# Kernel optimization log

Measured on AMD Instinct MI355X. Metric: run time of the kernel, lower is better.

The kernel has to match this reference:

```python
import jax, jax.numpy as jnp
import numpy as np

EPS = 1e-8
LAMBDA_LSE = 6.0
LAMBDA_SOFTMAX = 9.0
LEAKY_SLOPE = 0.1


def setup_inputs() -> dict:
    key = jax.random.key(0)
    k1, k2, k3 = jax.random.split(key, 3)
    images = jax.random.normal(k1, (128, 36, 512), dtype=jnp.float32)
    captions = jax.random.normal(k2, (64, 32, 512), dtype=jnp.float32)
    # caption lengths in [4, 32] so no caption is empty
    cap_lens = jax.random.randint(k3, (64,), 4, 33, dtype=jnp.int64)
    return {"images": images, "captions": captions, "cap_lens": cap_lens}


def reference(images, captions, cap_lens):
    """Vectorized xattn_score_t2i with raw_feature_norm='clipped_l2norm',
    agg_func='LogSumExp'. images: (I,R,D); captions: (C,L,D); cap_lens: (C,).
    Returns similarities (I, C), matching the torch per-caption loop.
    """
    C, L, D = captions.shape
    mask = jnp.arange(L)[None, :] < cap_lens[:, None]          # (C, L)

    # attn = bmm(context=images, query^T=words): (C, I, R, L)
    attn = jnp.einsum('ird,cld->cirl', images, captions)
    attn = jax.nn.leaky_relu(attn, LEAKY_SLOPE)
    # zero out padded words; equivalent to slicing caption to cap_len
    attn = attn * mask[:, None, None, :]
    # l2norm along the word dim (dim=2 of (I,R,L) in original)
    norm = jnp.sqrt(jnp.sum(attn * attn, axis=-1, keepdims=True)) + EPS
    attn = attn / norm

    # transpose -> (C, I, L, R); softmax over regions with smoothing
    attn = jnp.swapaxes(attn, -1, -2)
    attn = jax.nn.softmax(attn * LAMBDA_SOFTMAX, axis=-1)

    # weighted context: (C, I, L, D)
    wctx = jnp.einsum('cilr,ird->cild', attn, images)

    # cosine similarity between caption words and weighted context over D
    cap = captions[:, None, :, :]                               # (C, 1, L, D)
    num = jnp.sum(cap * wctx, axis=-1)                          # (C, I, L)
    den = (jnp.maximum(jnp.linalg.norm(cap, axis=-1), EPS) *
           jnp.maximum(jnp.linalg.norm(wctx, axis=-1), EPS))
    row_sim = num / den                                         # (C, I, L)

    # LogSumExp aggregation over valid words
    scores = jnp.where(mask[:, None, :], row_sim * LAMBDA_LSE, -jnp.inf)
    sims = jax.nn.logsumexp(scores, axis=-1) / LAMBDA_LSE       # (C, I)
    return sims.T                                               # (I, C)
```

## Files before the change

### kernel.cpp

```cpp
#include <hip/hip_runtime.h>
#include <math.h>

constexpr int In = 128, Rn = 36, Cn = 64, Ln = 32, Dn = 512;
constexpr int Mn = In * Rn;
constexpr int Nn = Cn * Ln;
constexpr size_t ABOFF = 0;
constexpr size_t BBOFF = (size_t)Mn * Dn / 2;
constexpr size_t GBOFF = BBOFF + (size_t)Nn * Dn / 2;
constexpr size_t CNOFF = GBOFF + (size_t)In * 48 * 64 / 2;
constexpr size_t WSFLOATS = CNOFF + (size_t)Cn * Ln;
constexpr float EPSf = 1e-8f, LLSE = 6.0f, LSM = 9.0f, SLOPE = 0.1f;

using short8 = __attribute__((ext_vector_type(8))) short;
using f32x4  = __attribute__((ext_vector_type(4))) float;

__device__ __forceinline__ float dot4(float4 a, float4 b) {
  return a.x * b.x + a.y * b.y + a.z * b.z + a.w * b.w;
}

__device__ __forceinline__ unsigned short f2bf(float x) {
  union { float f; unsigned u; } v; v.f = x;
  unsigned r = v.u + 0x7fffu + ((v.u >> 16) & 1u);
  return (unsigned short)(r >> 16);
}

__device__ __forceinline__ short8 pack8(float4 u, float4 v) {
  short8 s;
  s[0] = (short)f2bf(u.x); s[1] = (short)f2bf(u.y); s[2] = (short)f2bf(u.z); s[3] = (short)f2bf(u.w);
  s[4] = (short)f2bf(v.x); s[5] = (short)f2bf(v.y); s[6] = (short)f2bf(v.z); s[7] = (short)f2bf(v.w);
  return s;
}

extern "C" __global__ __launch_bounds__(256, 2)
void scan_pre(const float* __restrict__ images, const float* __restrict__ captions,
              float* __restrict__ ws)
{
  __shared__ unsigned short sI[48 * 520];
  const int tid = threadIdx.x;
  const int bx = blockIdx.x;
  const short8 z8 = {0, 0, 0, 0, 0, 0, 0, 0};

  if (bx < 128) {
    const int i = bx;
    const float* gi = images + (size_t)i * Rn * Dn;
    unsigned short* Ab = (unsigned short*)(ws + ABOFF) + (size_t)i * Rn * Dn;
    for (int q = 0; q < 9; ++q) {
      int ch = tid + q * 256;
      int r = ch >> 6, c8 = (ch & 63) * 8;
      float4 u = *reinterpret_cast<const float4*>(gi + r * Dn + c8);
      float4 v = *reinterpret_cast<const float4*>(gi + r * Dn + c8 + 4);
      short8 p = pack8(u, v);
      *reinterpret_cast<short8*>(Ab + r * Dn + c8) = p;
      *reinterpret_cast<short8*>(&sI[r * 520 + c8]) = p;
    }
    for (int q = 0; q < 3; ++q) {
      int ch = tid + q * 256;
      int r = 36 + (ch >> 6), c8 = (ch & 63) * 8;
      *reinterpret_cast<short8*>(&sI[r * 520 + c8]) = z8;
    }
    __syncthreads();
    const int lane = tid & 63, wv = tid >> 6;
    const int lr = lane & 15, lk = lane >> 4;
    unsigned short* gb = (unsigned short*)(ws + GBOFF) + (size_t)i * 48 * 64;
    for (int t = wv; t < 9; t += 4) {
      const int mt = t / 3, nt = t - mt * 3;
      f32x4 acc = {0.f, 0.f, 0.f, 0.f};
      for (int k = 0; k < 16; ++k) {
        short8 af = *reinterpret_cast<const short8*>(&sI[(mt * 16 + lr) * 520 + k * 32 + lk * 8]);
        short8 bf = *reinterpret_cast<const short8*>(&sI[(nt * 16 + lr) * 520 + k * 32 + lk * 8]);
        acc = __builtin_amdgcn_mfma_f32_16x16x32_bf16(af, bf, acc, 0, 0, 0);
      }
      #pragma unroll
      for (int j = 0; j < 4; ++j)
        gb[(mt * 16 + lk * 4 + j) * 64 + nt * 16 + lr] = f2bf(acc[j]);
    }
    if (tid < 96) {
      int r = tid >> 1, h = tid & 1;
      *reinterpret_cast<short8*>(gb + r * 64 + 48 + h * 8) = z8;
    }
    return;
  }
  if (bx < 640) {
    const int chunk = (bx - 128) * 256 + tid;
    unsigned short* Bbd = (unsigned short*)(ws + BBOFF);
    size_t off = (size_t)chunk * 8;
    float4 u = *reinterpret_cast<const float4*>(captions + off);
    float4 v = *reinterpret_cast<const float4*>(captions + off + 4);
    *reinterpret_cast<short8*>(Bbd + off) = pack8(u, v);
    return;
  }
  {
    const int c = bx - 640;
    const float* gc = captions + (size_t)c * Ln * Dn;
    const int l = tid >> 3, p = tid & 7;
    float s = 0.f;
    #pragma unroll
    for (int t = 0; t < 16; ++t) {
      float4 v = *reinterpret_cast<const float4*>(gc + l * Dn + p * 64 + t * 4);
      s += dot4(v, v);
    }
    s += __shfl_xor(s, 1, 64); s += __shfl_xor(s, 2, 64); s += __shfl_xor(s, 4, 64);
    if (p == 0) ws[CNOFF + c * Ln + l] = s;
  }
}

extern "C" __global__ __launch_bounds__(256, 2)
void scan_fused(const float* __restrict__ ws, const int* __restrict__ cap_lens,
                float* __restrict__ out)
{
  __shared__ unsigned short Al[48 * 72];
  __shared__ unsigned short Bl[128 * 72];
  const unsigned short* Ab = (const unsigned short*)(ws + ABOFF);
  const unsigned short* Bb = (const unsigned short*)(ws + BBOFF);
  const unsigned short* GbAll = (const unsigned short*)(ws + GBOFF);
  const float* cnArr = ws + CNOFF;

  const int tid = threadIdx.x;
  int bid = blockIdx.x;
  bid = (bid & 7) * 256 + (bid >> 3);
  const int ig = bid >> 4;
  const int cg = bid & 15;
  const int lane = tid & 63, wv = tid >> 6;
  const int lr = lane & 15, lk = lane >> 4;
  const int cap = cg * 4 + wv;
  const int len = cap_lens[cap];

  const int ar = tid >> 2, aq = tid & 3;
  const int br = tid >> 1, bh = tid & 1;

  const unsigned short* gA = Ab + ((size_t)ig * 36 + (ar < 36 ? ar : 0)) * Dn + aq * 16;
  const unsigned short* gB = Bb + ((size_t)(cg * 128) + br) * Dn + bh * 32;
  const bool aValid = (tid < 192) && (ar < 36);
  const bool aPad   = (tid < 192) && (ar >= 36);

  f32x4 acc[3][2];
  #pragma unroll
  for (int x = 0; x < 3; ++x)
    #pragma unroll
    for (int y = 0; y < 2; ++y) acc[x][y] = {0.f, 0.f, 0.f, 0.f};

  for (int k0 = 0; k0 < Dn; k0 += 64) {
    short8 a0 = {0,0,0,0,0,0,0,0}, a1 = {0,0,0,0,0,0,0,0};
    if (aValid) {
      a0 = *reinterpret_cast<const short8*>(gA + k0);
      a1 = *reinterpret_cast<const short8*>(gA + k0 + 8);
    }
    short8 b0 = *reinterpret_cast<const short8*>(gB + k0);
    short8 b1 = *reinterpret_cast<const short8*>(gB + k0 + 8);
    short8 b2 = *reinterpret_cast<const short8*>(gB + k0 + 16);
    short8 b3 = *reinterpret_cast<const short8*>(gB + k0 + 24);
    __syncthreads();
    if (aValid || aPad) {
      *reinterpret_cast<short8*>(&Al[ar * 72 + aq * 16])     = a0;
      *reinterpret_cast<short8*>(&Al[ar * 72 + aq * 16 + 8]) = a1;
    }
    {
      unsigned short* w = &Bl[br * 72 + bh * 32];
      *reinterpret_cast<short8*>(w)      = b0;
      *reinterpret_cast<short8*>(w + 8)  = b1;
      *reinterpret_cast<short8*>(w + 16) = b2;
      *reinterpret_cast<short8*>(w + 24) = b3;
    }
    __syncthreads();
    #pragma unroll
    for (int ks = 0; ks < 2; ++ks) {
      short8 af[3], bf[2];
      #pragma unroll
      for (int x = 0; x < 3; ++x)
        af[x] = *reinterpret_cast<const short8*>(&Al[(x * 16 + lr) * 72 + ks * 32 + lk * 8]);
      #pragma unroll
      for (int y = 0; y < 2; ++y)
        bf[y] = *reinterpret_cast<const short8*>(&Bl[(wv * 32 + y * 16 + lr) * 72 + ks * 32 + lk * 8]);
      #pragma unroll
      for (int x = 0; x < 3; ++x)
        #pragma unroll
        for (int y = 0; y < 2; ++y)
          acc[x][y] = __builtin_amdgcn_mfma_f32_16x16x32_bf16(af[x], bf[y], acc[x][y], 0, 0, 0);
    }
  }

  const unsigned short* Gb = GbAll + (size_t)ig * 48 * 64;
  short8 gfr[3][2];
  #pragma unroll
  for (int x = 0; x < 3; ++x)
    #pragma unroll
    for (int ks = 0; ks < 2; ++ks)
      gfr[x][ks] = *reinterpret_cast<const short8*>(Gb + (x * 16 + lr) * 64 + ks * 32 + lk * 8);
  const float cn0 = cnArr[cap * 32 + lr];
  const float cn1 = cnArr[cap * 32 + 16 + lr];

  float s[3][2][4];
  #pragma unroll
  for (int x = 0; x < 3; ++x)
    #pragma unroll
    for (int y = 0; y < 2; ++y) {
      const int l = y * 16 + lr;
      #pragma unroll
      for (int j = 0; j < 4; ++j) {
        float v = acc[x][y][j];
        v = v > 0.f ? v : SLOPE * v;
        if (l >= len) v = 0.f;
        s[x][y][j] = v;
      }
    }

  float zinv[3][4];
  #pragma unroll
  for (int x = 0; x < 3; ++x)
    #pragma unroll
    for (int j = 0; j < 4; ++j) {
      float t = s[x][0][j] * s[x][0][j] + s[x][1][j] * s[x][1][j];
      t += __shfl_xor(t, 1, 64); t += __shfl_xor(t, 2, 64);
      t += __shfl_xor(t, 4, 64); t += __shfl_xor(t, 8, 64);
      zinv[x][j] = LSM / (sqrtf(t) + EPSf);
    }

  const bool x2ok = (lk == 0);
  float mcol[2] = {-1e30f, -1e30f};
  #pragma unroll
  for (int x = 0; x < 3; ++x)
    #pragma unroll
    for (int y = 0; y < 2; ++y)
      #pragma unroll
      for (int j = 0; j < 4; ++j) {
        float zz = s[x][y][j] * zinv[x][j];
        s[x][y][j] = zz;
        if (x < 2 || x2ok) mcol[y] = fmaxf(mcol[y], zz);
      }
  #pragma unroll
  for (int y = 0; y < 2; ++y) {
    mcol[y] = fmaxf(mcol[y], __shfl_xor(mcol[y], 16, 64));
    mcol[y] = fmaxf(mcol[y], __shfl_xor(mcol[y], 32, 64));
  }

  float e[3][2][4];
  float esum[2] = {0.f, 0.f}, num[2] = {0.f, 0.f};
  #pragma unroll
  for (int x = 0; x < 3; ++x)
    #pragma unroll
    for (int y = 0; y < 2; ++y)
      #pragma unroll
      for (int j = 0; j < 4; ++j) {
        float ev = (x < 2 || x2ok) ? __expf(s[x][y][j] - mcol[y]) : 0.f;
        e[x][y][j] = ev;
        esum[y] += ev;
        num[y] = fmaf(ev, acc[x][y][j], num[y]);
      }
  #pragma unroll
  for (int y = 0; y < 2; ++y) {
    esum[y] += __shfl_xor(esum[y], 16, 64); esum[y] += __shfl_xor(esum[y], 32, 64);
    num[y]  += __shfl_xor(num[y], 16, 64);  num[y]  += __shfl_xor(num[y], 32, 64);
  }

  unsigned short* ET = &Bl[(wv * 32) * 72];
  {
    const int zl = lane >> 1, zs = lane & 1;
    short8 zero = {0,0,0,0,0,0,0,0};
    *reinterpret_cast<short8*>(&ET[zl * 72 + 48 + zs * 8]) = zero;
  }
  #pragma unroll
  for (int x = 0; x < 3; ++x)
    #pragma unroll
    for (int y = 0; y < 2; ++y)
      #pragma unroll
      for (int j = 0; j < 4; ++j)
        ET[(y * 16 + lr) * 72 + (x * 16 + lk * 4 + j)] = f2bf(e[x][y][j]);
  __syncthreads();

  f32x4 vac[3][2];
  #pragma unroll
  for (int x = 0; x < 3; ++x)
    #pragma unroll
    for (int y = 0; y < 2; ++y) vac[x][y] = {0.f, 0.f, 0.f, 0.f};
  #pragma unroll
  for (int ks = 0; ks < 2; ++ks) {
    short8 efr[2];
    #pragma unroll
    for (int y = 0; y < 2; ++y)
      efr[y] = *reinterpret_cast<const short8*>(&ET[(y * 16 + lr) * 72 + ks * 32 + lk * 8]);
    #pragma unroll
    for (int x = 0; x < 3; ++x)
      #pragma unroll
      for (int y = 0; y < 2; ++y)
        vac[x][y] = __builtin_amdgcn_mfma_f32_16x16x32_bf16(gfr[x][ks], efr[y], vac[x][y], 0, 0, 0);
  }
  float wn[2] = {0.f, 0.f};
  #pragma unroll
  for (int x = 0; x < 3; ++x)
    #pragma unroll
    for (int y = 0; y < 2; ++y)
      #pragma unroll
      for (int j = 0; j < 4; ++j)
        wn[y] = fmaf(e[x][y][j], vac[x][y][j], wn[y]);
  #pragma unroll
  for (int y = 0; y < 2; ++y) {
    wn[y] += __shfl_xor(wn[y], 16, 64); wn[y] += __shfl_xor(wn[y], 32, 64);
  }

  float sc[2];
  #pragma unroll
  for (int y = 0; y < 2; ++y) {
    const int l = y * 16 + lr;
    const float cn = y ? cn1 : cn0;
    float inv = 1.f / esum[y];
    float nm = num[y] * inv;
    float w = fmaxf(wn[y], 0.f) * inv * inv;
    float den = fmaxf(sqrtf(cn), EPSf) * fmaxf(sqrtf(w), EPSf);
    sc[y] = (l < len) ? (nm / den) * LLSE : -INFINITY;
  }
  float mx = fmaxf(sc[0], sc[1]);
  mx = fmaxf(mx, __shfl_xor(mx, 1, 64)); mx = fmaxf(mx, __shfl_xor(mx, 2, 64));
  mx = fmaxf(mx, __shfl_xor(mx, 4, 64)); mx = fmaxf(mx, __shfl_xor(mx, 8, 64));
  float ex = __expf(sc[0] - mx) + __expf(sc[1] - mx);
  ex += __shfl_xor(ex, 1, 64); ex += __shfl_xor(ex, 2, 64);
  ex += __shfl_xor(ex, 4, 64); ex += __shfl_xor(ex, 8, 64);
  if (lane == 0) out[ig * Cn + cap] = (mx + __logf(ex)) / LLSE;
}

extern "C" void kernel_launch(void* const* d_in, const int* in_sizes, int n_in,
                              void* d_out, int out_size, void* d_ws, size_t ws_size,
                              hipStream_t stream) {
  const float* images   = (const float*)d_in[0];
  const float* captions = (const float*)d_in[1];
  const int*   cap_lens = (const int*)d_in[2];
  float* out = (float*)d_out;
  float* ws  = (float*)d_ws;
  if (ws_size < WSFLOATS * sizeof(float)) return;

  hipLaunchKernelGGL(scan_pre, dim3(704), dim3(256), 0, stream,
                     images, captions, ws);
  hipLaunchKernelGGL(scan_fused, dim3(In * 16), dim3(256), 0, stream,
                     ws, cap_lens, out);
}
```

Before: 45.20 us.

## Double captions per block to 8 waves, sharing image tile across more captions

Each fused block now handles 8 captions (512 threads, 8 waves) instead of 4. The shared image-region tile is then reused across twice as many captions, and the number of blocks halves. This cuts redundant global loads of the image tile. Loop pointers are precomputed and incremented instead of recomputed per iteration. The trade-off is higher LDS use and register pressure per block with 512-thread launch bounds, which may lower occupancy, and each barrier now synchronizes more waves.

Measured after the change: 46.65 us. +3.2%, slower.

```diff
diff --git a/kernel.cpp b/kernel.cpp
--- a/kernel.cpp
+++ b/kernel.cpp
@@ -104,12 +104,12 @@
   }
 }
 
-extern "C" __global__ __launch_bounds__(256, 2)
+extern "C" __global__ __launch_bounds__(512, 2)
 void scan_fused(const float* __restrict__ ws, const int* __restrict__ cap_lens,
                 float* __restrict__ out)
 {
   __shared__ unsigned short Al[48 * 72];
-  __shared__ unsigned short Bl[128 * 72];
+  __shared__ unsigned short Bl[256 * 72];
   const unsigned short* Ab = (const unsigned short*)(ws + ABOFF);
   const unsigned short* Bb = (const unsigned short*)(ws + BBOFF);
   const unsigned short* GbAll = (const unsigned short*)(ws + GBOFF);
@@ -117,21 +117,25 @@
 
   const int tid = threadIdx.x;
   int bid = blockIdx.x;
-  bid = (bid & 7) * 256 + (bid >> 3);
-  const int ig = bid >> 4;
-  const int cg = bid & 15;
+  bid = (bid & 7) * 128 + (bid >> 3);
+  const int ig = bid >> 3;
+  const int cg = bid & 7;
   const int lane = tid & 63, wv = tid >> 6;
   const int lr = lane & 15, lk = lane >> 4;
-  const int cap = cg * 4 + wv;
+  const int cap = cg * 8 + wv;
   const int len = cap_lens[cap];
 
   const int ar = tid >> 2, aq = tid & 3;
-  const int br = tid >> 1, bh = tid & 1;
-
-  const unsigned short* gA = Ab + ((size_t)ig * 36 + (ar < 36 ? ar : 0)) * Dn + aq * 16;
-  const unsigned short* gB = Bb + ((size_t)(cg * 128) + br) * Dn + bh * 32;
   const bool aValid = (tid < 192) && (ar < 36);
   const bool aPad   = (tid < 192) && (ar >= 36);
+  const int br = tid >> 1, bh = tid & 1;
+
+  const unsigned short* gA = Ab + ((size_t)ig * 36 + (ar < 36 ? ar : 0)) * Dn + aq * 16;
+  const unsigned short* gB = Bb + ((size_t)(cg * 256) + br) * Dn + bh * 32;
+  unsigned short* wAp = &Al[ar * 72 + aq * 16];
+  unsigned short* wBp = &Bl[br * 72 + bh * 32];
+  const unsigned short* rA = &Al[lr * 72 + lk * 8];
+  const unsigned short* rB = &Bl[(wv * 32 + lr) * 72 + lk * 8];
 
   f32x4 acc[3][2];
   #pragma unroll
@@ -139,38 +143,39 @@
     #pragma unroll
     for (int y = 0; y < 2; ++y) acc[x][y] = {0.f, 0.f, 0.f, 0.f};
 
-  for (int k0 = 0; k0 < Dn; k0 += 64) {
-    short8 a0 = {0,0,0,0,0,0,0,0}, a1 = {0,0,0,0,0,0,0,0};
+  const short8 z8 = {0, 0, 0, 0, 0, 0, 0, 0};
+
+  for (int t = 0; t < 8; ++t) {
+    short8 a0 = z8, a1 = z8;
     if (aValid) {
-      a0 = *reinterpret_cast<const short8*>(gA + k0);
-      a1 = *reinterpret_cast<const short8*>(gA + k0 + 8);
-    }
-    short8 b0 = *reinterpret_cast<const short8*>(gB + k0);
-    short8 b1 = *reinterpret_cast<const short8*>(gB + k0 + 8);
-    short8 b2 = *reinterpret_cast<const short8*>(gB + k0 + 16);
-    short8 b3 = *reinterpret_cast<const short8*>(gB + k0 + 24);
+      a0 = *reinterpret_cast<const short8*>(gA);
+      a1 = *reinterpret_cast<const short8*>(gA + 8);
+      gA += 64;
+    }
+    short8 b0 = *reinterpret_cast<const short8*>(gB);
+    short8 b1 = *reinterpret_cast<const short8*>(gB + 8);
+    short8 b2 = *reinterpret_cast<const short8*>(gB + 16);
+    short8 b3 = *reinterpret_cast<const short8*>(gB + 24);
+    gB += 64;
     __syncthreads();
     if (aValid || aPad) {
-      *reinterpret_cast<short8*>(&Al[ar * 72 + aq * 16])     = a0;
-      *reinterpret_cast<short8*>(&Al[ar * 72 + aq * 16 + 8]) = a1;
-    }
-    {
-      unsigned short* w = &Bl[br * 72 + bh * 32];
-      *reinterpret_cast<short8*>(w)      = b0;
-      *reinterpret_cast<short8*>(w + 8)  = b1;
-      *reinterpret_cast<short8*>(w + 16) = b2;
-      *reinterpret_cast<short8*>(w + 24) = b3;
-    }
+      *reinterpret_cast<short8*>(wAp)     = a0;
+      *reinterpret_cast<short8*>(wAp + 8) = a1;
+    }
+    *reinterpret_cast<short8*>(wBp)      = b0;
+    *reinterpret_cast<short8*>(wBp + 8)  = b1;
+    *reinterpret_cast<short8*>(wBp + 16) = b2;
+    *reinterpret_cast<short8*>(wBp + 24) = b3;
     __syncthreads();
     #pragma unroll
     for (int ks = 0; ks < 2; ++ks) {
       short8 af[3], bf[2];
       #pragma unroll
       for (int x = 0; x < 3; ++x)
-        af[x] = *reinterpret_cast<const short8*>(&Al[(x * 16 + lr) * 72 + ks * 32 + lk * 8]);
+        af[x] = *reinterpret_cast<const short8*>(rA + x * 16 * 72 + ks * 32);
       #pragma unroll
       for (int y = 0; y < 2; ++y)
-        bf[y] = *reinterpret_cast<const short8*>(&Bl[(wv * 32 + y * 16 + lr) * 72 + ks * 32 + lk * 8]);
+        bf[y] = *reinterpret_cast<const short8*>(rB + y * 16 * 72 + ks * 32);
       #pragma unroll
       for (int x = 0; x < 3; ++x)
         #pragma unroll
@@ -255,8 +260,7 @@
   unsigned short* ET = &Bl[(wv * 32) * 72];
   {
     const int zl = lane >> 1, zs = lane & 1;
-    short8 zero = {0,0,0,0,0,0,0,0};
-    *reinterpret_cast<short8*>(&ET[zl * 72 + 48 + zs * 8]) = zero;
+    *reinterpret_cast<short8*>(&ET[zl * 72 + 48 + zs * 8]) = z8;
   }
   #pragma unroll
   for (int x = 0; x < 3; ++x)
@@ -329,6 +333,6 @@
 
   hipLaunchKernelGGL(scan_pre, dim3(704), dim3(256), 0, stream,
                      images, captions, ws);
-  hipLaunchKernelGGL(scan_fused, dim3(In * 16), dim3(256), 0, stream,
+  hipLaunchKernelGGL(scan_fused, dim3(In * 8), dim3(512), 0, stream,
                      ws, cap_lens, out);
 }
```

## Double-buffer LDS tiles in scan_fused GEMM loop to overlap loads with MFMA

Applied to the files above, without the earlier changes.

The shared-memory A and B tiles are double-buffered, and the K loop is restructured: the first tile is preloaded, then each iteration issues global loads for the next tile before running the MFMAs on the current buffer. The loaded data is written to the other buffer afterwards, which cuts the barriers from two per iteration to one and hides global latency behind compute. The padded A rows are zeroed once in both buffers. The barrier before the per-wave ET staging is also removed, since each wave only reads its own region. LDS use per block roughly doubles, which could limit occupancy.

Result: slower. 48.34 us (+6.9%).

```diff
diff --git a/kernel.cpp b/kernel.cpp
--- a/kernel.cpp
+++ b/kernel.cpp
@@ -108,8 +108,8 @@
 void scan_fused(const float* __restrict__ ws, const int* __restrict__ cap_lens,
                 float* __restrict__ out)
 {
-  __shared__ unsigned short Al[48 * 72];
-  __shared__ unsigned short Bl[128 * 72];
+  __shared__ unsigned short Al[2][48 * 72];
+  __shared__ unsigned short Bl[2][128 * 72];
   const unsigned short* Ab = (const unsigned short*)(ws + ABOFF);
   const unsigned short* Bb = (const unsigned short*)(ws + BBOFF);
   const unsigned short* GbAll = (const unsigned short*)(ws + GBOFF);
@@ -126,12 +126,15 @@
   const int len = cap_lens[cap];
 
   const int ar = tid >> 2, aq = tid & 3;
+  const bool aValid = (tid < 192) && (ar < 36);
+  const bool aPad   = (tid < 192) && (ar >= 36);
   const int br = tid >> 1, bh = tid & 1;
 
   const unsigned short* gA = Ab + ((size_t)ig * 36 + (ar < 36 ? ar : 0)) * Dn + aq * 16;
   const unsigned short* gB = Bb + ((size_t)(cg * 128) + br) * Dn + bh * 32;
-  const bool aValid = (tid < 192) && (ar < 36);
-  const bool aPad   = (tid < 192) && (ar >= 36);
+  const int aOff = ar * 72 + aq * 16;
+  const int bOff = br * 72 + bh * 32;
+  const short8 z8 = {0, 0, 0, 0, 0, 0, 0, 0};
 
   f32x4 acc[3][2];
   #pragma unroll
@@ -139,43 +142,69 @@
     #pragma unroll
     for (int y = 0; y < 2; ++y) acc[x][y] = {0.f, 0.f, 0.f, 0.f};
 
-  for (int k0 = 0; k0 < Dn; k0 += 64) {
-    short8 a0 = {0,0,0,0,0,0,0,0}, a1 = {0,0,0,0,0,0,0,0};
+  {
     if (aValid) {
-      a0 = *reinterpret_cast<const short8*>(gA + k0);
-      a1 = *reinterpret_cast<const short8*>(gA + k0 + 8);
-    }
-    short8 b0 = *reinterpret_cast<const short8*>(gB + k0);
-    short8 b1 = *reinterpret_cast<const short8*>(gB + k0 + 8);
-    short8 b2 = *reinterpret_cast<const short8*>(gB + k0 + 16);
-    short8 b3 = *reinterpret_cast<const short8*>(gB + k0 + 24);
-    __syncthreads();
-    if (aValid || aPad) {
-      *reinterpret_cast<short8*>(&Al[ar * 72 + aq * 16])     = a0;
-      *reinterpret_cast<short8*>(&Al[ar * 72 + aq * 16 + 8]) = a1;
-    }
-    {
-      unsigned short* w = &Bl[br * 72 + bh * 32];
-      *reinterpret_cast<short8*>(w)      = b0;
-      *reinterpret_cast<short8*>(w + 8)  = b1;
-      *reinterpret_cast<short8*>(w + 16) = b2;
-      *reinterpret_cast<short8*>(w + 24) = b3;
-    }
-    __syncthreads();
+      *reinterpret_cast<short8*>(&Al[0][aOff])     = *reinterpret_cast<const short8*>(gA);
+      *reinterpret_cast<short8*>(&Al[0][aOff + 8]) = *reinterpret_cast<const short8*>(gA + 8);
+      gA += 64;
+    } else if (aPad) {
+      *reinterpret_cast<short8*>(&Al[0][aOff])     = z8;
+      *reinterpret_cast<short8*>(&Al[0][aOff + 8]) = z8;
+      *reinterpret_cast<short8*>(&Al[1][aOff])     = z8;
+      *reinterpret_cast<short8*>(&Al[1][aOff + 8]) = z8;
+    }
+    unsigned short* w = &Bl[0][bOff];
+    *reinterpret_cast<short8*>(w)      = *reinterpret_cast<const short8*>(gB);
+    *reinterpret_cast<short8*>(w + 8)  = *reinterpret_cast<const short8*>(gB + 8);
+    *reinterpret_cast<short8*>(w + 16) = *reinterpret_cast<const short8*>(gB + 16);
+    *reinterpret_cast<short8*>(w + 24) = *reinterpret_cast<const short8*>(gB + 24);
+    gB += 64;
+  }
+  __syncthreads();
+
+  for (int t = 0; t < 8; ++t) {
+    const int cur = t & 1, nxt = cur ^ 1;
+    short8 a0n, a1n, b0n, b1n, b2n, b3n;
+    if (t < 7) {
+      if (aValid) {
+        a0n = *reinterpret_cast<const short8*>(gA);
+        a1n = *reinterpret_cast<const short8*>(gA + 8);
+        gA += 64;
+      }
+      b0n = *reinterpret_cast<const short8*>(gB);
+      b1n = *reinterpret_cast<const short8*>(gB + 8);
+      b2n = *reinterpret_cast<const short8*>(gB + 16);
+      b3n = *reinterpret_cast<const short8*>(gB + 24);
+      gB += 64;
+    }
+    const unsigned short* rA = &Al[cur][lr * 72 + lk * 8];
+    const unsigned short* rB = &Bl[cur][(wv * 32 + lr) * 72 + lk * 8];
     #pragma unroll
     for (int ks = 0; ks < 2; ++ks) {
       short8 af[3], bf[2];
       #pragma unroll
       for (int x = 0; x < 3; ++x)
-        af[x] = *reinterpret_cast<const short8*>(&Al[(x * 16 + lr) * 72 + ks * 32 + lk * 8]);
+        af[x] = *reinterpret_cast<const short8*>(rA + x * 16 * 72 + ks * 32);
       #pragma unroll
       for (int y = 0; y < 2; ++y)
-        bf[y] = *reinterpret_cast<const short8*>(&Bl[(wv * 32 + y * 16 + lr) * 72 + ks * 32 + lk * 8]);
+        bf[y] = *reinterpret_cast<const short8*>(rB + y * 16 * 72 + ks * 32);
       #pragma unroll
       for (int x = 0; x < 3; ++x)
         #pragma unroll
         for (int y = 0; y < 2; ++y)
           acc[x][y] = __builtin_amdgcn_mfma_f32_16x16x32_bf16(af[x], bf[y], acc[x][y], 0, 0, 0);
+    }
+    if (t < 7) {
+      if (aValid) {
+        *reinterpret_cast<short8*>(&Al[nxt][aOff])     = a0n;
+        *reinterpret_cast<short8*>(&Al[nxt][aOff + 8]) = a1n;
+      }
+      unsigned short* w = &Bl[nxt][bOff];
+      *reinterpret_cast<short8*>(w)      = b0n;
+      *reinterpret_cast<short8*>(w + 8)  = b1n;
+      *reinterpret_cast<short8*>(w + 16) = b2n;
+      *reinterpret_cast<short8*>(w + 24) = b3n;
+      __syncthreads();
     }
   }
 
@@ -252,11 +281,10 @@
     num[y]  += __shfl_xor(num[y], 16, 64);  num[y]  += __shfl_xor(num[y], 32, 64);
   }
 
-  unsigned short* ET = &Bl[(wv * 32) * 72];
+  unsigned short* ET = &Bl[0][(wv * 32) * 72];
   {
     const int zl = lane >> 1, zs = lane & 1;
-    short8 zero = {0,0,0,0,0,0,0,0};
-    *reinterpret_cast<short8*>(&ET[zl * 72 + 48 + zs * 8]) = zero;
+    *reinterpret_cast<short8*>(&ET[zl * 72 + 48 + zs * 8]) = z8;
   }
   #pragma unroll
   for (int x = 0; x < 3; ++x)
@@ -265,7 +293,6 @@
       #pragma unroll
       for (int j = 0; j < 4; ++j)
         ET[(y * 16 + lr) * 72 + (x * 16 + lk * 4 + j)] = f2bf(e[x][y][j]);
-  __syncthreads();
 
   f32x4 vac[3][2];
   #pragma unroll
```

## Pre-pack captions into MFMA fragment order and stream B straight to registers

Applied to the files above, without the earlier changes.

The caption conversion pass now writes bf16 captions in per-lane MFMA fragment order. The fused kernel can then load B fragments straight from global memory into registers, with a one-step register prefetch, instead of staging them through LDS. The whole 36x512 image tile (padded to 48 rows) is loaded into LDS once, which removes the two barriers per K step. The softmax-weights scratch reuses the pad rows of that tile, and occupancy is raised to 3 blocks per CU. The trade-offs are higher register pressure from the prefetch buffers, a large LDS allocation per block, and the ET reads for ks=1 now running past each 48-wide row; this stays harmless only because the matching G columns are zero.

Result: faster. 42.95 us (-5.0%).

```diff
diff --git a/kernel.cpp b/kernel.cpp
--- a/kernel.cpp
+++ b/kernel.cpp
@@ -82,11 +82,20 @@
   }
   if (bx < 640) {
     const int chunk = (bx - 128) * 256 + tid;
-    unsigned short* Bbd = (unsigned short*)(ws + BBOFF);
-    size_t off = (size_t)chunk * 8;
-    float4 u = *reinterpret_cast<const float4*>(captions + off);
-    float4 v = *reinterpret_cast<const float4*>(captions + off + 4);
-    *reinterpret_cast<short8*>(Bbd + off) = pack8(u, v);
+    const int c  = chunk >> 11;
+    const int cc = chunk & 2047;
+    const int ln = cc & 63;
+    const int fc = cc >> 6;
+    const int t  = fc >> 2;
+    const int ks = (fc >> 1) & 1;
+    const int y  = fc & 1;
+    const int lr = ln & 15, lk = ln >> 4;
+    const float* src = captions + ((size_t)c * Ln + y * 16 + lr) * Dn
+                     + t * 64 + ks * 32 + lk * 8;
+    float4 u = *reinterpret_cast<const float4*>(src);
+    float4 v = *reinterpret_cast<const float4*>(src + 4);
+    unsigned short* dst = (unsigned short*)(ws + BBOFF) + (size_t)chunk * 8;
+    *reinterpret_cast<short8*>(dst) = pack8(u, v);
     return;
   }
   {
@@ -104,14 +113,13 @@
   }
 }
 
-extern "C" __global__ __launch_bounds__(256, 2)
+extern "C" __global__ __launch_bounds__(256, 3)
 void scan_fused(const float* __restrict__ ws, const int* __restrict__ cap_lens,
                 float* __restrict__ out)
 {
-  __shared__ unsigned short Al[48 * 72];
-  __shared__ unsigned short Bl[128 * 72];
+  __shared__ unsigned short sA[48 * 520];
   const unsigned short* Ab = (const unsigned short*)(ws + ABOFF);
-  const unsigned short* Bb = (const unsigned short*)(ws + BBOFF);
+  const unsigned short* Bf = (const unsigned short*)(ws + BBOFF);
   const unsigned short* GbAll = (const unsigned short*)(ws + GBOFF);
   const float* cnArr = ws + CNOFF;
 
@@ -124,14 +132,28 @@
   const int lr = lane & 15, lk = lane >> 4;
   const int cap = cg * 4 + wv;
   const int len = cap_lens[cap];
-
-  const int ar = tid >> 2, aq = tid & 3;
-  const int br = tid >> 1, bh = tid & 1;
-
-  const unsigned short* gA = Ab + ((size_t)ig * 36 + (ar < 36 ? ar : 0)) * Dn + aq * 16;
-  const unsigned short* gB = Bb + ((size_t)(cg * 128) + br) * Dn + bh * 32;
-  const bool aValid = (tid < 192) && (ar < 36);
-  const bool aPad   = (tid < 192) && (ar >= 36);
+  const short8 z8 = {0, 0, 0, 0, 0, 0, 0, 0};
+
+  {
+    const unsigned short* Abi = Ab + (size_t)ig * (Rn * Dn);
+    #pragma unroll
+    for (int q = 0; q < 9; ++q) {
+      int ch = tid + q * 256;
+      int r = ch >> 6, c8 = (ch & 63) * 8;
+      *reinterpret_cast<short8*>(&sA[r * 520 + c8]) =
+        *reinterpret_cast<const short8*>(Abi + r * Dn + c8);
+    }
+    #pragma unroll
+    for (int q = 0; q < 3; ++q) {
+      int ch = tid + q * 256;
+      int r = 36 + (ch >> 6), c8 = (ch & 63) * 8;
+      *reinterpret_cast<short8*>(&sA[r * 520 + c8]) = z8;
+    }
+  }
+  __syncthreads();
+
+  const unsigned short* gBp = Bf + (size_t)cap * 16384 + lane * 8;
+  const unsigned short* rA = &sA[lr * 520 + lk * 8];
 
   f32x4 acc[3][2];
   #pragma unroll
@@ -139,43 +161,33 @@
     #pragma unroll
     for (int y = 0; y < 2; ++y) acc[x][y] = {0.f, 0.f, 0.f, 0.f};
 
-  for (int k0 = 0; k0 < Dn; k0 += 64) {
-    short8 a0 = {0,0,0,0,0,0,0,0}, a1 = {0,0,0,0,0,0,0,0};
-    if (aValid) {
-      a0 = *reinterpret_cast<const short8*>(gA + k0);
-      a1 = *reinterpret_cast<const short8*>(gA + k0 + 8);
-    }
-    short8 b0 = *reinterpret_cast<const short8*>(gB + k0);
-    short8 b1 = *reinterpret_cast<const short8*>(gB + k0 + 8);
-    short8 b2 = *reinterpret_cast<const short8*>(gB + k0 + 16);
-    short8 b3 = *reinterpret_cast<const short8*>(gB + k0 + 24);
-    __syncthreads();
-    if (aValid || aPad) {
-      *reinterpret_cast<short8*>(&Al[ar * 72 + aq * 16])     = a0;
-      *reinterpret_cast<short8*>(&Al[ar * 72 + aq * 16 + 8]) = a1;
-    }
-    {
-      unsigned short* w = &Bl[br * 72 + bh * 32];
-      *reinterpret_cast<short8*>(w)      = b0;
-      *reinterpret_cast<short8*>(w + 8)  = b1;
-      *reinterpret_cast<short8*>(w + 16) = b2;
-      *reinterpret_cast<short8*>(w + 24) = b3;
-    }
-    __syncthreads();
+  short8 bc[4], bn[4];
+  #pragma unroll
+  for (int f = 0; f < 4; ++f)
+    bc[f] = *reinterpret_cast<const short8*>(gBp + f * 512);
+
+  #pragma unroll 2
+  for (int t = 0; t < 8; ++t) {
+    if (t < 7) {
+      #pragma unroll
+      for (int f = 0; f < 4; ++f)
+        bn[f] = *reinterpret_cast<const short8*>(gBp + (t + 1) * 2048 + f * 512);
+    }
     #pragma unroll
     for (int ks = 0; ks < 2; ++ks) {
-      short8 af[3], bf[2];
+      short8 af[3];
       #pragma unroll
       for (int x = 0; x < 3; ++x)
-        af[x] = *reinterpret_cast<const short8*>(&Al[(x * 16 + lr) * 72 + ks * 32 + lk * 8]);
-      #pragma unroll
-      for (int y = 0; y < 2; ++y)
-        bf[y] = *reinterpret_cast<const short8*>(&Bl[(wv * 32 + y * 16 + lr) * 72 + ks * 32 + lk * 8]);
+        af[x] = *reinterpret_cast<const short8*>(rA + x * 8320 + t * 64 + ks * 32);
       #pragma unroll
       for (int x = 0; x < 3; ++x)
         #pragma unroll
         for (int y = 0; y < 2; ++y)
-          acc[x][y] = __builtin_amdgcn_mfma_f32_16x16x32_bf16(af[x], bf[y], acc[x][y], 0, 0, 0);
+          acc[x][y] = __builtin_amdgcn_mfma_f32_16x16x32_bf16(af[x], bc[ks * 2 + y], acc[x][y], 0, 0, 0);
+    }
+    if (t < 7) {
+      #pragma unroll
+      for (int f = 0; f < 4; ++f) bc[f] = bn[f];
     }
   }
 
@@ -252,20 +264,15 @@
     num[y]  += __shfl_xor(num[y], 16, 64);  num[y]  += __shfl_xor(num[y], 32, 64);
   }
 
-  unsigned short* ET = &Bl[(wv * 32) * 72];
-  {
-    const int zl = lane >> 1, zs = lane & 1;
-    short8 zero = {0,0,0,0,0,0,0,0};
-    *reinterpret_cast<short8*>(&ET[zl * 72 + 48 + zs * 8]) = zero;
-  }
+  __syncthreads();
+  unsigned short* ET = &sA[36 * 520 + wv * 1552];
   #pragma unroll
   for (int x = 0; x < 3; ++x)
     #pragma unroll
     for (int y = 0; y < 2; ++y)
       #pragma unroll
       for (int j = 0; j < 4; ++j)
-        ET[(y * 16 + lr) * 72 + (x * 16 + lk * 4 + j)] = f2bf(e[x][y][j]);
-  __syncthreads();
+        ET[(y * 16 + lr) * 48 + (x * 16 + lk * 4 + j)] = f2bf(e[x][y][j]);
 
   f32x4 vac[3][2];
   #pragma unroll
@@ -277,7 +284,7 @@
     short8 efr[2];
     #pragma unroll
     for (int y = 0; y < 2; ++y)
-      efr[y] = *reinterpret_cast<const short8*>(&ET[(y * 16 + lr) * 72 + ks * 32 + lk * 8]);
+      efr[y] = *reinterpret_cast<const short8*>(&ET[(y * 16 + lr) * 48 + ks * 32 + lk * 8]);
     #pragma unroll
     for (int x = 0; x < 3; ++x)
       #pragma unroll
```
